# Kernel optimization log

Measured on AMD Instinct MI355X. Metric: run time of the kernel, lower is better.

Reference implementation:

```python
import jax, jax.numpy as jnp
import numpy as np

B, C, T, H = 2, 1024, 2048, 16
D = C // H  # head dim = 64


def setup_inputs() -> dict:
    key = jax.random.key(0)
    ks = jax.random.split(key, 10)
    s = 1.0 / np.sqrt(C).astype(np.float32)
    x = jax.random.normal(ks[0], (B, C, T), jnp.float32)
    mask = jax.random.randint(ks[1], (B, 1, T), 0, 2).astype(bool)
    Wq = jax.random.normal(ks[2], (C, C), jnp.float32) * s
    bq = jax.random.normal(ks[3], (C,), jnp.float32) * 0.02
    Wk = jax.random.normal(ks[4], (C, C), jnp.float32) * s
    bk = jax.random.normal(ks[5], (C,), jnp.float32) * 0.02
    Wv = jax.random.normal(ks[6], (C, C), jnp.float32) * s
    bv = jax.random.normal(ks[7], (C,), jnp.float32) * 0.02
    Wp = jax.random.normal(ks[8], (C, C), jnp.float32) * s
    bp = jax.random.normal(ks[9], (C,), jnp.float32) * 0.02
    return {"x": x, "mask": mask, "Wq": Wq, "bq": bq, "Wk": Wk, "bk": bk,
            "Wv": Wv, "bv": bv, "Wp": Wp, "bp": bp}


def _conv1x1(W, b, z):
    # Conv1d with kernel size 1 == per-position GEMM over channels.
    return jnp.einsum('oc,bct->bot', W, z) + b[None, :, None]


def reference(x, mask, Wq, bq, Wk, bk, Wv, bv, Wp, bp):
    b_, c_, t_ = x.shape
    scale = 1.0 / np.sqrt(D).astype(np.float32)
    q = _conv1x1(Wq, bq, x)
    k = _conv1x1(Wk, bk, x)
    v = _conv1x1(Wv, bv, x)
    # [B, C, T] -> [B, H, T, D]  (view(B,H,D,T).transpose(2,3))
    q = q.reshape(b_, H, D, t_).transpose(0, 1, 3, 2)
    k = k.reshape(b_, H, D, t_).transpose(0, 1, 3, 2)
    v = v.reshape(b_, H, D, t_).transpose(0, 1, 3, 2)
    att = jnp.einsum('bhqd,bhkd->bhqk', q * scale, k)
    m = mask[:, :, None, :]  # [B,1,1,T] key mask
    att = jnp.where(m, att, -jnp.inf)
    p = jax.nn.softmax(att, axis=-1)
    p = jnp.where(m, p, 0.0)
    vm = v * mask[:, :, :, None].astype(v.dtype)  # zero masked values
    out = jnp.einsum('bhqk,bhkd->bhqd', p, vm)
    # [B,H,T,D] -> [B,C,T]
    out = out.transpose(0, 1, 3, 2).reshape(b_, c_, t_)
    out = _conv1x1(Wp, bp, out) * mask.astype(out.dtype)
    return (out, mask)
```

## Files before the change

kernel.cpp:

```cpp
#include <hip/hip_runtime.h>

typedef unsigned short u16;
typedef unsigned int u32;
typedef short bf16x8 __attribute__((ext_vector_type(8)));
typedef float f32x4 __attribute__((ext_vector_type(4)));

constexpr int Bb = 2, Cc = 1024, Tt = 2048, Hh = 16, Dd = 64;

__device__ __forceinline__ u16 f2bf(float f) {
    union { float f; u32 i; } c; c.f = f;
    u32 u = c.i;
    u32 r = (u + 0x7FFFu + ((u >> 16) & 1u)) >> 16;
    return (u16)r;
}
__device__ __forceinline__ u32 pk_bf2(float lo, float hi) {
    union { float f; u32 i; } a, b; a.f = lo; b.f = hi;
    u32 ua = a.i + 0x8000u, ub = b.i + 0x8000u;
    return (ub & 0xFFFF0000u) | (ua >> 16);
}
__device__ __forceinline__ u32 scl2(u32 w) {
    union { float f; u32 i; } lo, hi;
    lo.i = w << 16; hi.i = w & 0xFFFF0000u;
    lo.f *= 0.125f; hi.f *= 0.125f;
    return (hi.i & 0xFFFF0000u) | (lo.i >> 16);
}
__device__ __forceinline__ void gl_lds16(const u16* g, u16* l) {
    __builtin_amdgcn_global_load_lds(
        (const __attribute__((address_space(1))) u32*)(const void*)g,
        (__attribute__((address_space(3))) u32*)(void*)l, 16, 0, 0);
}

__global__ __launch_bounds__(256) void scan_mask(const int* __restrict__ mask,
                                                 int* __restrict__ pfx,
                                                 int* __restrict__ tmap,
                                                 int* __restrict__ nk) {
    __shared__ int part[256];
    int b = blockIdx.x;
    const int* m = mask + b * Tt;
    int t8 = threadIdx.x * 8;
    int v[8], s = 0;
#pragma unroll
    for (int i = 0; i < 8; i++) { v[i] = m[t8 + i] ? 1 : 0; s += v[i]; }
    part[threadIdx.x] = s;
    __syncthreads();
    for (int off = 1; off < 256; off <<= 1) {
        int val = (threadIdx.x >= off) ? part[threadIdx.x - off] : 0;
        __syncthreads();
        part[threadIdx.x] += val;
        __syncthreads();
    }
    int run = part[threadIdx.x] - s;
#pragma unroll
    for (int i = 0; i < 8; i++) {
        pfx[b * Tt + t8 + i] = run;
        if (v[i]) { tmap[b * Tt + run] = t8 + i; run++; }
    }
    if (threadIdx.x == 255) nk[b] = part[255];
}

__global__ __launch_bounds__(256) void cvt_w4(const float* __restrict__ w0,
                                              const float* __restrict__ w1,
                                              const float* __restrict__ w2,
                                              const float* __restrict__ w3,
                                              u16* __restrict__ out) {
    int wsel = blockIdx.y;
    const float* in = (wsel == 0) ? w0 : (wsel == 1) ? w1 : (wsel == 2) ? w2 : w3;
    u16* o = out + (size_t)wsel * Cc * Cc;
    int i = (blockIdx.x * 256 + threadIdx.x) * 4;
    float4 v = *(const float4*)(in + i);
    o[i + 0] = f2bf(v.x);
    o[i + 1] = f2bf(v.y);
    o[i + 2] = f2bf(v.z);
    o[i + 3] = f2bf(v.w);
}

__global__ __launch_bounds__(256) void transpose_x(const float* __restrict__ x,
                                                   const int* __restrict__ mask,
                                                   const int* __restrict__ pfx,
                                                   u16* __restrict__ xT) {
    __shared__ u16 tile[32][33];
    int b = blockIdx.z;
    int t0 = blockIdx.x * 32, c0 = blockIdx.y * 32;
    int tx = threadIdx.x, ty = threadIdx.y;
    const float* xb = x + (size_t)b * Cc * Tt;
    u16* xTb = xT + (size_t)b * Tt * Cc;
#pragma unroll
    for (int i = 0; i < 4; i++) {
        int r = ty + i * 8;
        tile[r][tx] = f2bf(xb[(size_t)(c0 + r) * Tt + t0 + tx]);
    }
    __syncthreads();
#pragma unroll
    for (int i = 0; i < 4; i++) {
        int r = ty + i * 8;
        int t = t0 + r;
        if (mask[b * Tt + t]) {
            int slot = pfx[b * Tt + t];
            xTb[(size_t)slot * Cc + c0 + tx] = tile[tx][r];
        }
    }
}

__global__ __launch_bounds__(256) void gemm_qkv(const u16* __restrict__ A,
                                                const u16* __restrict__ Bt,
                                                const float* __restrict__ b0,
                                                const float* __restrict__ b1,
                                                const float* __restrict__ b2,
                                                const int* __restrict__ nk,
                                                u16* __restrict__ qb, u16* __restrict__ kb,
                                                u16* __restrict__ vT) {
    constexpr int K = Cc;
    __shared__ u16 Alds[128 * 64];
    __shared__ u16 Blds[128 * 64];
    int n0 = blockIdx.x * 128, m0 = blockIdx.y * 128;
    int bb = m0 >> 11;
    if ((m0 & 2047) >= nk[bb]) return;
    int tid = threadIdx.x;
    int lane = tid & 63, wave = tid >> 6;
    int quad = lane >> 4, id15 = lane & 15;
    int wm0 = (wave & 1) * 64, wn0 = (wave >> 1) * 64;
    int srow = lane >> 3;
    int scol = ((lane & 7) ^ srow) * 8;
    int sw = id15 & 7;

    f32x4 acc[4][4] = {};

    for (int k0 = 0; k0 < K; k0 += 64) {
        __syncthreads();
#pragma unroll
        for (int t = 0; t < 4; t++) {
            int g = wave * 4 + t;
            int r = g * 8 + srow;
            gl_lds16(A + (size_t)(m0 + r) * K + k0 + scol, &Alds[g * 512]);
            gl_lds16(Bt + (size_t)(n0 + r) * K + k0 + scol, &Blds[g * 512]);
        }
        __syncthreads();
#pragma unroll
        for (int hf = 0; hf < 2; hf++) {
            bf16x8 af[4], bf[4];
#pragma unroll
            for (int i = 0; i < 4; i++) {
                int c = (((hf << 2) | quad) ^ sw) * 8;
                af[i] = *(const bf16x8*)(&Alds[(wm0 + i * 16 + id15) * 64 + c]);
                bf[i] = *(const bf16x8*)(&Blds[(wn0 + i * 16 + id15) * 64 + c]);
            }
#pragma unroll
            for (int ni = 0; ni < 4; ni++)
#pragma unroll
                for (int mi = 0; mi < 4; mi++)
                    acc[ni][mi] = __builtin_amdgcn_mfma_f32_16x16x32_bf16(
                        bf[ni], af[mi], acc[ni][mi], 0, 0, 0);
        }
    }

    int mt0 = (m0 & 2047) + wm0;
#pragma unroll
    for (int ni = 0; ni < 4; ni++) {
        int nr = n0 + wn0 + ni * 16 + quad * 4;
        int sect = nr >> 10;
        int nn = nr & 1023;
        int h = nn >> 6, d0 = nn & 63;
        const float* bp_ = (sect == 0) ? b0 : (sect == 1) ? b1 : b2;
        float4 bv4 = *(const float4*)(bp_ + nn);
        if (sect < 2) {
            u16* dst = ((sect == 0) ? qb : kb) + ((size_t)bb * Hh + h) * Tt * (size_t)Dd;
#pragma unroll
            for (int mi = 0; mi < 4; mi++) {
                int mt = mt0 + mi * 16 + id15;
                uint2 w;
                w.x = pk_bf2(acc[ni][mi][0] + bv4.x, acc[ni][mi][1] + bv4.y);
                w.y = pk_bf2(acc[ni][mi][2] + bv4.z, acc[ni][mi][3] + bv4.w);
                *(uint2*)(dst + (size_t)mt * Dd + d0) = w;
            }
        } else {
            u16* dst = vT + ((size_t)bb * Hh + h) * Dd * (size_t)Tt;
#pragma unroll
            for (int mi = 0; mi < 4; mi++) {
                int mt = mt0 + mi * 16 + id15;
                dst[(size_t)(d0 + 0) * Tt + mt] = f2bf(acc[ni][mi][0] + bv4.x);
                dst[(size_t)(d0 + 1) * Tt + mt] = f2bf(acc[ni][mi][1] + bv4.y);
                dst[(size_t)(d0 + 2) * Tt + mt] = f2bf(acc[ni][mi][2] + bv4.z);
                dst[(size_t)(d0 + 3) * Tt + mt] = f2bf(acc[ni][mi][3] + bv4.w);
            }
        }
    }
}

__global__ __launch_bounds__(256) void gemm_proj(const u16* __restrict__ A,
                                                 const u16* __restrict__ Bt,
                                                 const float* __restrict__ b0,
                                                 const int* __restrict__ mask,
                                                 float* __restrict__ out) {
    constexpr int K = Cc;
    __shared__ u16 Alds[128 * 64];
    __shared__ u16 Blds[64 * 64];
    int n0 = blockIdx.x * 64, m0 = blockIdx.y * 128;
    int tid = threadIdx.x;
    int lane = tid & 63, wave = tid >> 6;
    int quad = lane >> 4, id15 = lane & 15;
    int wn0 = (wave & 1) * 32, wm0 = (wave >> 1) * 64;
    int srow = lane >> 3;
    int scol = ((lane & 7) ^ srow) * 8;
    int sw = id15 & 7;

    f32x4 acc[2][4] = {};

    for (int k0 = 0; k0 < K; k0 += 64) {
        __syncthreads();
#pragma unroll
        for (int t = 0; t < 4; t++) {
            int g = wave * 4 + t;
            gl_lds16(A + (size_t)(m0 + g * 8 + srow) * K + k0 + scol, &Alds[g * 512]);
        }
#pragma unroll
        for (int t = 0; t < 2; t++) {
            int g = wave * 2 + t;
            gl_lds16(Bt + (size_t)(n0 + g * 8 + srow) * K + k0 + scol, &Blds[g * 512]);
        }
        __syncthreads();
#pragma unroll
        for (int hf = 0; hf < 2; hf++) {
            bf16x8 af[4], bf[2];
            int c = (((hf << 2) | quad) ^ sw) * 8;
#pragma unroll
            for (int i = 0; i < 4; i++)
                af[i] = *(const bf16x8*)(&Alds[(wm0 + i * 16 + id15) * 64 + c]);
#pragma unroll
            for (int i = 0; i < 2; i++)
                bf[i] = *(const bf16x8*)(&Blds[(wn0 + i * 16 + id15) * 64 + c]);
#pragma unroll
            for (int ni = 0; ni < 2; ni++)
#pragma unroll
                for (int mi = 0; mi < 4; mi++)
                    acc[ni][mi] = __builtin_amdgcn_mfma_f32_16x16x32_bf16(
                        bf[ni], af[mi], acc[ni][mi], 0, 0, 0);
        }
    }

    int bb = m0 >> 11;
    int mt0 = (m0 & 2047) + wm0;
#pragma unroll
    for (int ni = 0; ni < 2; ni++) {
        int nr = n0 + wn0 + ni * 16 + quad * 4;
        float4 bv4 = *(const float4*)(b0 + nr);
#pragma unroll
        for (int mi = 0; mi < 4; mi++) {
            int m = mt0 + mi * 16 + id15;
            int mg = (bb << 11) + m;
            float mm = (float)mask[mg];
            float* o = out + ((size_t)bb * Cc + nr) * Tt + m;
            o[0 * Tt] = (acc[ni][mi][0] + bv4.x) * mm;
            o[1 * Tt] = (acc[ni][mi][1] + bv4.y) * mm;
            o[2 * Tt] = (acc[ni][mi][2] + bv4.z) * mm;
            o[3 * Tt] = (acc[ni][mi][3] + bv4.w) * mm;
        }
    }
}

__global__ __launch_bounds__(256) void attn(const u16* __restrict__ q,
                                            const u16* __restrict__ kk,
                                            const u16* __restrict__ vT,
                                            const int* __restrict__ tmap,
                                            const int* __restrict__ nk,
                                            u16* __restrict__ o_buf) {
    __shared__ u16 Kl[2][128 * 64];
    __shared__ u16 Vl[2][64 * 128];
    int bh = blockIdx.y;
    int b = bh >> 4, h = bh & 15;
    int t0 = blockIdx.x * 128;
    int nkb = nk[b];
    if (t0 >= nkb) return;
    int tid = threadIdx.x;
    int lane = tid & 63, wave = tid >> 6;
    int quad = lane >> 4, id15 = lane & 15;
    int wq = t0 + wave * 32;
    const u16* qb = q + (size_t)bh * Tt * Dd;
    const u16* kb = kk + (size_t)bh * Tt * Dd;
    const u16* vb = vT + (size_t)bh * Dd * Tt;

    union { uint4 r; bf16x8 v; } qf[2][2];
#pragma unroll
    for (int qg = 0; qg < 2; qg++)
#pragma unroll
        for (int hf = 0; hf < 2; hf++) {
            uint4 r = *(const uint4*)(qb + (size_t)(wq + qg * 16 + id15) * Dd +
                                      hf * 32 + quad * 8);
            qf[qg][hf].r.x = scl2(r.x);
            qf[qg][hf].r.y = scl2(r.y);
            qf[qg][hf].r.z = scl2(r.z);
            qf[qg][hf].r.w = scl2(r.w);
        }

    int srowK = lane >> 3;
    int scolK = ((lane & 7) ^ srowK) * 8;
    int srowV = lane >> 4;
    int sw = id15 & 7;

    float l[2] = {0.0f, 0.0f};
    f32x4 accO[4][2] = {};

#pragma unroll
    for (int t = 0; t < 4; t++) {
        int g = wave * 4 + t;
        gl_lds16(kb + (size_t)(g * 8 + srowK) * Dd + scolK, &Kl[0][g * 512]);
        int d = g * 4 + srowV;
        int sc = (lane & 15) ^ (4 * (g & 1) + srowV);
        gl_lds16(vb + (size_t)d * Tt + sc * 8, &Vl[0][g * 512]);
    }

    int shA = ((quad & 1) * 2) * 16 + id15;
    int shB = shA + 16;

    int cbuf = 0;
    for (int j0 = 0; j0 < nkb; j0 += 128, cbuf ^= 1) {
        __syncthreads();
        if (j0 + 128 < nkb) {
            int bb = cbuf ^ 1, jn = j0 + 128;
#pragma unroll
            for (int t = 0; t < 4; t++) {
                int g = wave * 4 + t;
                gl_lds16(kb + (size_t)(jn + g * 8 + srowK) * Dd + scolK, &Kl[bb][g * 512]);
                int d = g * 4 + srowV;
                int sc = (lane & 15) ^ (4 * (g & 1) + srowV);
                gl_lds16(vb + (size_t)d * Tt + jn + sc * 8, &Vl[bb][g * 512]);
            }
        }
        const u16* Kb = Kl[cbuf];
        const u16* Vb = Vl[cbuf];

        f32x4 st[8][2] = {};
#pragma unroll
        for (int kt = 0; kt < 8; kt++) {
            int krow = kt * 16 + id15;
#pragma unroll
            for (int hf = 0; hf < 2; hf++) {
                bf16x8 kf = *(const bf16x8*)(Kb + krow * 64 + (((hf << 2) | quad) ^ sw) * 8);
                st[kt][0] = __builtin_amdgcn_mfma_f32_16x16x32_bf16(kf, qf[0][hf].v, st[kt][0], 0, 0, 0);
                st[kt][1] = __builtin_amdgcn_mfma_f32_16x16x32_bf16(kf, qf[1][hf].v, st[kt][1], 0, 0, 0);
            }
        }

        if (j0 + 128 > nkb) {
#pragma unroll
            for (int kt = 0; kt < 8; kt++) {
                int jb = j0 + kt * 16 + quad * 4;
#pragma unroll
                for (int qg = 0; qg < 2; qg++)
#pragma unroll
                    for (int r = 0; r < 4; r++)
                        if (jb + r >= nkb) st[kt][qg][r] = -1e30f;
            }
        }

        u32 pkk[4][2][2][2];
#pragma unroll
        for (int kt = 0; kt < 8; kt++) {
#pragma unroll
            for (int qg = 0; qg < 2; qg++) {
                float p0 = __expf(st[kt][qg][0]);
                float p1 = __expf(st[kt][qg][1]);
                float p2 = __expf(st[kt][qg][2]);
                float p3 = __expf(st[kt][qg][3]);
                l[qg] += (p0 + p1) + (p2 + p3);
                pkk[kt >> 1][qg][kt & 1][0] = pk_bf2(p0, p1);
                pkk[kt >> 1][qg][kt & 1][1] = pk_bf2(p2, p3);
            }
        }

#pragma unroll
        for (int g = 0; g < 4; g++) {
            union { u32 u[4]; bf16x8 v; } pf[2];
#pragma unroll
            for (int qg = 0; qg < 2; qg++) {
                u32 a0 = (u32)__shfl((int)pkk[g][qg][0][0], shA);
                u32 a1 = (u32)__shfl((int)pkk[g][qg][0][1], shA);
                u32 a2 = (u32)__shfl((int)pkk[g][qg][0][0], shB);
                u32 a3 = (u32)__shfl((int)pkk[g][qg][0][1], shB);
                u32 c0 = (u32)__shfl((int)pkk[g][qg][1][0], shA);
                u32 c1 = (u32)__shfl((int)pkk[g][qg][1][1], shA);
                u32 c2 = (u32)__shfl((int)pkk[g][qg][1][0], shB);
                u32 c3 = (u32)__shfl((int)pkk[g][qg][1][1], shB);
                pf[qg].u[0] = (quad < 2) ? a0 : c0;
                pf[qg].u[1] = (quad < 2) ? a1 : c1;
                pf[qg].u[2] = (quad < 2) ? a2 : c2;
                pf[qg].u[3] = (quad < 2) ? a3 : c3;
            }
#pragma unroll
            for (int dt = 0; dt < 4; dt++) {
                int drow = dt * 16 + id15;
                bf16x8 vf = *(const bf16x8*)(Vb + drow * 128 + (((g << 2) | quad) ^ sw) * 8);
                accO[dt][0] = __builtin_amdgcn_mfma_f32_16x16x32_bf16(vf, pf[0].v, accO[dt][0], 0, 0, 0);
                accO[dt][1] = __builtin_amdgcn_mfma_f32_16x16x32_bf16(vf, pf[1].v, accO[dt][1], 0, 0, 0);
            }
        }
    }

#pragma unroll
    for (int qg = 0; qg < 2; qg++) {
        int slot = wq + qg * 16 + id15;
        bool ok = slot < nkb;
        int torig = ok ? tmap[b * Tt + slot] : 0;
        float lv = l[qg];
        lv += __shfl_xor(lv, 16);
        lv += __shfl_xor(lv, 32);
        float inv = 1.0f / lv;
        if (ok) {
#pragma unroll
            for (int dt = 0; dt < 4; dt++) {
                uint2 w;
                w.x = pk_bf2(accO[dt][qg][0] * inv, accO[dt][qg][1] * inv);
                w.y = pk_bf2(accO[dt][qg][2] * inv, accO[dt][qg][3] * inv);
                *(uint2*)(o_buf + ((size_t)b * Tt + torig) * Cc + h * Dd +
                          dt * 16 + quad * 4) = w;
            }
        }
    }
}

__global__ void mask_out_k(const int* __restrict__ mask, float* __restrict__ out) {
    int i = blockIdx.x * 256 + threadIdx.x;
    if (i < Bb * Tt) out[i] = mask[i] ? 1.0f : 0.0f;
}

extern "C" void kernel_launch(void* const* d_in, const int* in_sizes, int n_in,
                              void* d_out, int out_size, void* d_ws, size_t ws_size,
                              hipStream_t stream) {
    const float* x  = (const float*)d_in[0];
    const int* mask = (const int*)d_in[1];
    const float* Wq = (const float*)d_in[2];
    const float* bq = (const float*)d_in[3];
    const float* Wk = (const float*)d_in[4];
    const float* bk = (const float*)d_in[5];
    const float* Wv = (const float*)d_in[6];
    const float* bv = (const float*)d_in[7];
    const float* Wp = (const float*)d_in[8];
    const float* bp = (const float*)d_in[9];
    float* out = (float*)d_out;

    size_t sz = (size_t)Bb * Tt * Cc;
    size_t wsz = (size_t)Cc * Cc;
    u16* xT = (u16*)d_ws;
    u16* qb = xT + sz;
    u16* kb = qb + sz;
    u16* vT = kb + sz;
    u16* wq16 = vT + sz;
    u16* wp16 = wq16 + 3 * wsz;
    int* pfx  = (int*)(wp16 + wsz);
    int* tmap = pfx + Bb * Tt;
    int* nkp  = tmap + Bb * Tt;
    u16* ob = xT;

    scan_mask<<<Bb, 256, 0, stream>>>(mask, pfx, tmap, nkp);
    cvt_w4<<<dim3((int)(wsz / 1024), 4), 256, 0, stream>>>(Wq, Wk, Wv, Wp, wq16);
    transpose_x<<<dim3(Tt / 32, Cc / 32, Bb), dim3(32, 8), 0, stream>>>(x, mask, pfx, xT);
    gemm_qkv<<<dim3(3 * Cc / 128, Bb * Tt / 128), 256, 0, stream>>>(
        xT, wq16, bq, bk, bv, nkp, qb, kb, vT);
    attn<<<dim3(Tt / 128, Bb * Hh), 256, 0, stream>>>(qb, kb, vT, tmap, nkp, ob);
    gemm_proj<<<dim3(Cc / 64, Bb * Tt / 128), 256, 0, stream>>>(ob, wp16, bp, mask, out);
    if (out_size >= Bb * Cc * Tt + Bb * Tt)
        mask_out_k<<<dim3((Bb * Tt + 255) / 256), 256, 0, stream>>>(
            mask, out + (size_t)Bb * Cc * Tt);
}
```

Before: 184.8 us.

## Halve attention query tile, merge prep kernels, fold mask output into projection

The attention kernel now gives each wave one 16-row query group instead of two, so each block covers 64 query slots and the grid doubles. This raises block count and occupancy for the compacted key sequence, at the cost of loading each K/V tile twice as often per query. The mask scan and weight conversion are merged into one launch, and the mask tail output is written by the first block of the projection GEMM, which removes two kernel launches.

```diff
diff --git a/kernel.cpp b/kernel.cpp
--- a/kernel.cpp
+++ b/kernel.cpp
@@ -30,48 +30,50 @@
         (__attribute__((address_space(3))) u32*)(void*)l, 16, 0, 0);
 }
 
-__global__ __launch_bounds__(256) void scan_mask(const int* __restrict__ mask,
-                                                 int* __restrict__ pfx,
-                                                 int* __restrict__ tmap,
-                                                 int* __restrict__ nk) {
-    __shared__ int part[256];
-    int b = blockIdx.x;
-    const int* m = mask + b * Tt;
-    int t8 = threadIdx.x * 8;
-    int v[8], s = 0;
-#pragma unroll
-    for (int i = 0; i < 8; i++) { v[i] = m[t8 + i] ? 1 : 0; s += v[i]; }
-    part[threadIdx.x] = s;
-    __syncthreads();
-    for (int off = 1; off < 256; off <<= 1) {
-        int val = (threadIdx.x >= off) ? part[threadIdx.x - off] : 0;
-        __syncthreads();
-        part[threadIdx.x] += val;
-        __syncthreads();
-    }
-    int run = part[threadIdx.x] - s;
-#pragma unroll
-    for (int i = 0; i < 8; i++) {
-        pfx[b * Tt + t8 + i] = run;
-        if (v[i]) { tmap[b * Tt + run] = t8 + i; run++; }
-    }
-    if (threadIdx.x == 255) nk[b] = part[255];
-}
-
-__global__ __launch_bounds__(256) void cvt_w4(const float* __restrict__ w0,
-                                              const float* __restrict__ w1,
-                                              const float* __restrict__ w2,
-                                              const float* __restrict__ w3,
-                                              u16* __restrict__ out) {
-    int wsel = blockIdx.y;
-    const float* in = (wsel == 0) ? w0 : (wsel == 1) ? w1 : (wsel == 2) ? w2 : w3;
-    u16* o = out + (size_t)wsel * Cc * Cc;
-    int i = (blockIdx.x * 256 + threadIdx.x) * 4;
-    float4 v = *(const float4*)(in + i);
-    o[i + 0] = f2bf(v.x);
-    o[i + 1] = f2bf(v.y);
-    o[i + 2] = f2bf(v.z);
-    o[i + 3] = f2bf(v.w);
+__global__ __launch_bounds__(256) void prep(const int* __restrict__ mask,
+                                            int* __restrict__ pfx,
+                                            int* __restrict__ tmap,
+                                            int* __restrict__ nk,
+                                            const float* __restrict__ w0,
+                                            const float* __restrict__ w1,
+                                            const float* __restrict__ w2,
+                                            const float* __restrict__ w3,
+                                            u16* __restrict__ wout) {
+    if (blockIdx.x < 2) {
+        __shared__ int part[256];
+        int b = blockIdx.x;
+        const int* m = mask + b * Tt;
+        int t8 = threadIdx.x * 8;
+        int v[8], s = 0;
+#pragma unroll
+        for (int i = 0; i < 8; i++) { v[i] = m[t8 + i] ? 1 : 0; s += v[i]; }
+        part[threadIdx.x] = s;
+        __syncthreads();
+        for (int off = 1; off < 256; off <<= 1) {
+            int val = (threadIdx.x >= off) ? part[threadIdx.x - off] : 0;
+            __syncthreads();
+            part[threadIdx.x] += val;
+            __syncthreads();
+        }
+        int run = part[threadIdx.x] - s;
+#pragma unroll
+        for (int i = 0; i < 8; i++) {
+            pfx[b * Tt + t8 + i] = run;
+            if (v[i]) { tmap[b * Tt + run] = t8 + i; run++; }
+        }
+        if (threadIdx.x == 255) nk[b] = part[255];
+    } else {
+        int bi = blockIdx.x - 2;
+        int wsel = bi >> 10, blk = bi & 1023;
+        const float* in = (wsel == 0) ? w0 : (wsel == 1) ? w1 : (wsel == 2) ? w2 : w3;
+        u16* o = wout + (size_t)wsel * Cc * Cc;
+        int i = (blk * 256 + threadIdx.x) * 4;
+        float4 v = *(const float4*)(in + i);
+        o[i + 0] = f2bf(v.x);
+        o[i + 1] = f2bf(v.y);
+        o[i + 2] = f2bf(v.z);
+        o[i + 3] = f2bf(v.w);
+    }
 }
 
 __global__ __launch_bounds__(256) void transpose_x(const float* __restrict__ x,
@@ -190,12 +192,16 @@
                                                  const u16* __restrict__ Bt,
                                                  const float* __restrict__ b0,
                                                  const int* __restrict__ mask,
-                                                 float* __restrict__ out) {
+                                                 float* __restrict__ out,
+                                                 float* __restrict__ outTail) {
     constexpr int K = Cc;
     __shared__ u16 Alds[128 * 64];
     __shared__ u16 Blds[64 * 64];
     int n0 = blockIdx.x * 64, m0 = blockIdx.y * 128;
     int tid = threadIdx.x;
+    if (outTail && blockIdx.x == 0 && blockIdx.y == 0) {
+        for (int i = tid; i < Bb * Tt; i += 256) outTail[i] = mask[i] ? 1.0f : 0.0f;
+    }
     int lane = tid & 63, wave = tid >> 6;
     int quad = lane >> 4, id15 = lane & 15;
     int wn0 = (wave & 1) * 32, wm0 = (wave >> 1) * 64;
@@ -267,37 +273,34 @@
     __shared__ u16 Vl[2][64 * 128];
     int bh = blockIdx.y;
     int b = bh >> 4, h = bh & 15;
-    int t0 = blockIdx.x * 128;
+    int t0 = blockIdx.x * 64;
     int nkb = nk[b];
     if (t0 >= nkb) return;
     int tid = threadIdx.x;
     int lane = tid & 63, wave = tid >> 6;
     int quad = lane >> 4, id15 = lane & 15;
-    int wq = t0 + wave * 32;
+    int wq = t0 + wave * 16;
     const u16* qb = q + (size_t)bh * Tt * Dd;
     const u16* kb = kk + (size_t)bh * Tt * Dd;
     const u16* vb = vT + (size_t)bh * Dd * Tt;
 
-    union { uint4 r; bf16x8 v; } qf[2][2];
-#pragma unroll
-    for (int qg = 0; qg < 2; qg++)
-#pragma unroll
-        for (int hf = 0; hf < 2; hf++) {
-            uint4 r = *(const uint4*)(qb + (size_t)(wq + qg * 16 + id15) * Dd +
-                                      hf * 32 + quad * 8);
-            qf[qg][hf].r.x = scl2(r.x);
-            qf[qg][hf].r.y = scl2(r.y);
-            qf[qg][hf].r.z = scl2(r.z);
-            qf[qg][hf].r.w = scl2(r.w);
-        }
+    union { uint4 r; bf16x8 v; } qf[2];
+#pragma unroll
+    for (int hf = 0; hf < 2; hf++) {
+        uint4 r = *(const uint4*)(qb + (size_t)(wq + id15) * Dd + hf * 32 + quad * 8);
+        qf[hf].r.x = scl2(r.x);
+        qf[hf].r.y = scl2(r.y);
+        qf[hf].r.z = scl2(r.z);
+        qf[hf].r.w = scl2(r.w);
+    }
 
     int srowK = lane >> 3;
     int scolK = ((lane & 7) ^ srowK) * 8;
     int srowV = lane >> 4;
     int sw = id15 & 7;
 
-    float l[2] = {0.0f, 0.0f};
-    f32x4 accO[4][2] = {};
+    float l = 0.0f;
+    f32x4 accO[4] = {};
 
 #pragma unroll
     for (int t = 0; t < 4; t++) {
@@ -315,28 +318,27 @@
     for (int j0 = 0; j0 < nkb; j0 += 128, cbuf ^= 1) {
         __syncthreads();
         if (j0 + 128 < nkb) {
-            int bb = cbuf ^ 1, jn = j0 + 128;
+            int bn = cbuf ^ 1, jn = j0 + 128;
 #pragma unroll
             for (int t = 0; t < 4; t++) {
                 int g = wave * 4 + t;
-                gl_lds16(kb + (size_t)(jn + g * 8 + srowK) * Dd + scolK, &Kl[bb][g * 512]);
+                gl_lds16(kb + (size_t)(jn + g * 8 + srowK) * Dd + scolK, &Kl[bn][g * 512]);
                 int d = g * 4 + srowV;
                 int sc = (lane & 15) ^ (4 * (g & 1) + srowV);
-                gl_lds16(vb + (size_t)d * Tt + jn + sc * 8, &Vl[bb][g * 512]);
+                gl_lds16(vb + (size_t)d * Tt + jn + sc * 8, &Vl[bn][g * 512]);
             }
         }
         const u16* Kb = Kl[cbuf];
         const u16* Vb = Vl[cbuf];
 
-        f32x4 st[8][2] = {};
+        f32x4 st[8] = {};
 #pragma unroll
         for (int kt = 0; kt < 8; kt++) {
             int krow = kt * 16 + id15;
 #pragma unroll
             for (int hf = 0; hf < 2; hf++) {
                 bf16x8 kf = *(const bf16x8*)(Kb + krow * 64 + (((hf << 2) | quad) ^ sw) * 8);
-                st[kt][0] = __builtin_amdgcn_mfma_f32_16x16x32_bf16(kf, qf[0][hf].v, st[kt][0], 0, 0, 0);
-                st[kt][1] = __builtin_amdgcn_mfma_f32_16x16x32_bf16(kf, qf[1][hf].v, st[kt][1], 0, 0, 0);
+                st[kt] = __builtin_amdgcn_mfma_f32_16x16x32_bf16(kf, qf[hf].v, st[kt], 0, 0, 0);
             }
         }
 
@@ -345,81 +347,63 @@
             for (int kt = 0; kt < 8; kt++) {
                 int jb = j0 + kt * 16 + quad * 4;
 #pragma unroll
-                for (int qg = 0; qg < 2; qg++)
-#pragma unroll
-                    for (int r = 0; r < 4; r++)
-                        if (jb + r >= nkb) st[kt][qg][r] = -1e30f;
-            }
-        }
-
-        u32 pkk[4][2][2][2];
+                for (int r = 0; r < 4; r++)
+                    if (jb + r >= nkb) st[kt][r] = -1e30f;
+            }
+        }
+
+        u32 pkk[4][2][2];
 #pragma unroll
         for (int kt = 0; kt < 8; kt++) {
-#pragma unroll
-            for (int qg = 0; qg < 2; qg++) {
-                float p0 = __expf(st[kt][qg][0]);
-                float p1 = __expf(st[kt][qg][1]);
-                float p2 = __expf(st[kt][qg][2]);
-                float p3 = __expf(st[kt][qg][3]);
-                l[qg] += (p0 + p1) + (p2 + p3);
-                pkk[kt >> 1][qg][kt & 1][0] = pk_bf2(p0, p1);
-                pkk[kt >> 1][qg][kt & 1][1] = pk_bf2(p2, p3);
-            }
+            float p0 = __expf(st[kt][0]);
+            float p1 = __expf(st[kt][1]);
+            float p2 = __expf(st[kt][2]);
+            float p3 = __expf(st[kt][3]);
+            l += (p0 + p1) + (p2 + p3);
+            pkk[kt >> 1][kt & 1][0] = pk_bf2(p0, p1);
+            pkk[kt >> 1][kt & 1][1] = pk_bf2(p2, p3);
         }
 
 #pragma unroll
         for (int g = 0; g < 4; g++) {
-            union { u32 u[4]; bf16x8 v; } pf[2];
-#pragma unroll
-            for (int qg = 0; qg < 2; qg++) {
-                u32 a0 = (u32)__shfl((int)pkk[g][qg][0][0], shA);
-                u32 a1 = (u32)__shfl((int)pkk[g][qg][0][1], shA);
-                u32 a2 = (u32)__shfl((int)pkk[g][qg][0][0], shB);
-                u32 a3 = (u32)__shfl((int)pkk[g][qg][0][1], shB);
-                u32 c0 = (u32)__shfl((int)pkk[g][qg][1][0], shA);
-                u32 c1 = (u32)__shfl((int)pkk[g][qg][1][1], shA);
-                u32 c2 = (u32)__shfl((int)pkk[g][qg][1][0], shB);
-                u32 c3 = (u32)__shfl((int)pkk[g][qg][1][1], shB);
-                pf[qg].u[0] = (quad < 2) ? a0 : c0;
-                pf[qg].u[1] = (quad < 2) ? a1 : c1;
-                pf[qg].u[2] = (quad < 2) ? a2 : c2;
-                pf[qg].u[3] = (quad < 2) ? a3 : c3;
-            }
+            union { u32 u[4]; bf16x8 v; } pf;
+            u32 a0 = (u32)__shfl((int)pkk[g][0][0], shA);
+            u32 a1 = (u32)__shfl((int)pkk[g][0][1], shA);
+            u32 a2 = (u32)__shfl((int)pkk[g][0][0], shB);
+            u32 a3 = (u32)__shfl((int)pkk[g][0][1], shB);
+            u32 c0 = (u32)__shfl((int)pkk[g][1][0], shA);
+            u32 c1 = (u32)__shfl((int)pkk[g][1][1], shA);
+            u32 c2 = (u32)__shfl((int)pkk[g][1][0], shB);
+            u32 c3 = (u32)__shfl((int)pkk[g][1][1], shB);
+            pf.u[0] = (quad < 2) ? a0 : c0;
+            pf.u[1] = (quad < 2) ? a1 : c1;
+            pf.u[2] = (quad < 2) ? a2 : c2;
+            pf.u[3] = (quad < 2) ? a3 : c3;
 #pragma unroll
             for (int dt = 0; dt < 4; dt++) {
                 int drow = dt * 16 + id15;
                 bf16x8 vf = *(const bf16x8*)(Vb + drow * 128 + (((g << 2) | quad) ^ sw) * 8);
-                accO[dt][0] = __builtin_amdgcn_mfma_f32_16x16x32_bf16(vf, pf[0].v, accO[dt][0], 0, 0, 0);
-                accO[dt][1] = __builtin_amdgcn_mfma_f32_16x16x32_bf16(vf, pf[1].v, accO[dt][1], 0, 0, 0);
-            }
-        }
-    }
-
-#pragma unroll
-    for (int qg = 0; qg < 2; qg++) {
-        int slot = wq + qg * 16 + id15;
-        bool ok = slot < nkb;
-        int torig = ok ? tmap[b * Tt + slot] : 0;
-        float lv = l[qg];
-        lv += __shfl_xor(lv, 16);
-        lv += __shfl_xor(lv, 32);
-        float inv = 1.0f / lv;
-        if (ok) {
-#pragma unroll
-            for (int dt = 0; dt < 4; dt++) {
-                uint2 w;
-                w.x = pk_bf2(accO[dt][qg][0] * inv, accO[dt][qg][1] * inv);
-                w.y = pk_bf2(accO[dt][qg][2] * inv, accO[dt][qg][3] * inv);
-                *(uint2*)(o_buf + ((size_t)b * Tt + torig) * Cc + h * Dd +
-                          dt * 16 + quad * 4) = w;
-            }
-        }
-    }
-}
-
-__global__ void mask_out_k(const int* __restrict__ mask, float* __restrict__ out) {
-    int i = blockIdx.x * 256 + threadIdx.x;
-    if (i < Bb * Tt) out[i] = mask[i] ? 1.0f : 0.0f;
+                accO[dt] = __builtin_amdgcn_mfma_f32_16x16x32_bf16(vf, pf.v, accO[dt], 0, 0, 0);
+            }
+        }
+    }
+
+    int slot = wq + id15;
+    bool ok = slot < nkb;
+    int torig = ok ? tmap[b * Tt + slot] : 0;
+    float lv = l;
+    lv += __shfl_xor(lv, 16);
+    lv += __shfl_xor(lv, 32);
+    float inv = 1.0f / lv;
+    if (ok) {
+#pragma unroll
+        for (int dt = 0; dt < 4; dt++) {
+            uint2 w;
+            w.x = pk_bf2(accO[dt][0] * inv, accO[dt][1] * inv);
+            w.y = pk_bf2(accO[dt][2] * inv, accO[dt][3] * inv);
+            *(uint2*)(o_buf + ((size_t)b * Tt + torig) * Cc + h * Dd + dt * 16 + quad * 4) = w;
+        }
+    }
 }
 
 extern "C" void kernel_launch(void* const* d_in, const int* in_sizes, int n_in,
@@ -450,14 +434,15 @@
     int* nkp  = tmap + Bb * Tt;
     u16* ob = xT;
 
-    scan_mask<<<Bb, 256, 0, stream>>>(mask, pfx, tmap, nkp);
-    cvt_w4<<<dim3((int)(wsz / 1024), 4), 256, 0, stream>>>(Wq, Wk, Wv, Wp, wq16);
+    float* outTail = (out_size >= Bb * Cc * Tt + Bb * Tt)
+                         ? out + (size_t)Bb * Cc * Tt : nullptr;
+
+    prep<<<2 + 4 * (int)(wsz / 1024), 256, 0, stream>>>(
+        mask, pfx, tmap, nkp, Wq, Wk, Wv, Wp, wq16);
     transpose_x<<<dim3(Tt / 32, Cc / 32, Bb), dim3(32, 8), 0, stream>>>(x, mask, pfx, xT);
     gemm_qkv<<<dim3(3 * Cc / 128, Bb * Tt / 128), 256, 0, stream>>>(
         xT, wq16, bq, bk, bv, nkp, qb, kb, vT);
-    attn<<<dim3(Tt / 128, Bb * Hh), 256, 0, stream>>>(qb, kb, vT, tmap, nkp, ob);
-    gemm_proj<<<dim3(Cc / 64, Bb * Tt / 128), 256, 0, stream>>>(ob, wp16, bp, mask, out);
-    if (out_size >= Bb * Cc * Tt + Bb * Tt)
-        mask_out_k<<<dim3((Bb * Tt + 255) / 256), 256, 0, stream>>>(
-            mask, out + (size_t)Bb * Cc * Tt);
-}
+    attn<<<dim3(Tt / 64, Bb * Hh), 256, 0, stream>>>(qb, kb, vT, tmap, nkp, ob);
+    gemm_proj<<<dim3(Cc / 64, Bb * Tt / 128), 256, 0, stream>>>(
+        ob, wp16, bp, mask, out, outTail);
+}
```

After: 186.6 us. Within noise of the previous version (+0.9%).
